# Optimization experiments

Measured on AMD Instinct MI355X. Metric: run time of the kernel, lower is better.

Reference implementation:

```python
import jax, jax.numpy as jnp
import numpy as np

HEADS = 8
NEG = -1e9
EPS = 1e-9


def setup_inputs() -> dict:
    key = jax.random.key(0)
    ks = jax.random.split(key, 24)
    N, D, E = 2048, 512, 64
    s = 0.02
    inp = {
        "xyz": jax.random.normal(ks[0], (N, 3), jnp.float32),
        "str_feat": jax.random.normal(ks[1], (N, D), jnp.float32),
        "esm_feat": jax.random.normal(ks[2], (N, E), jnp.float32),
        "y_hat": jax.random.uniform(ks[3], (N, 1), jnp.float32),
        "distance_mask": jax.random.randint(ks[4], (N, N), 0, 2, jnp.int32),
        "t": jnp.ones((1,), jnp.float32),
        "band_width": jnp.ones((1,), jnp.float32),
        "max_iter": 5,
        # main projections (torch Linear layout: y = x @ W.T + b)
        "Wq": jax.random.normal(ks[5], (D, D), jnp.float32) * s,
        "bq": jnp.zeros((D,), jnp.float32),
        "Wk": jax.random.normal(ks[6], (D, D), jnp.float32) * s,
        "bk": jnp.zeros((D,), jnp.float32),
        "Wv": jax.random.normal(ks[7], (D, D), jnp.float32) * s,
        "bv": jnp.zeros((D,), jnp.float32),
        "Wo": jax.random.normal(ks[8], (D, D), jnp.float32) * s,
        "bo": jnp.zeros((D,), jnp.float32),
        # esm projections (computed in the original forward but unused downstream)
        "Weq": jax.random.normal(ks[9], (E, E), jnp.float32) * s,
        "beq": jnp.zeros((E,), jnp.float32),
        "Wek": jax.random.normal(ks[10], (E, E), jnp.float32) * s,
        "bek": jnp.zeros((E,), jnp.float32),
        "Wev": jax.random.normal(ks[11], (E, E), jnp.float32) * s,
        "bev": jnp.zeros((E,), jnp.float32),
        "Weo": jax.random.normal(ks[12], (E, E), jnp.float32) * s,
        "beo": jnp.zeros((E,), jnp.float32),
    }
    return inp


def reference(xyz, str_feat, esm_feat, y_hat, distance_mask, t, band_width, max_iter,
              Wq, bq, Wk, bk, Wv, bv, Wo, bo,
              Weq, beq, Wek, bek, Wev, bev, Weo, beo):
    N, D = str_feat.shape
    h = HEADS
    dh = D // h

    q = str_feat @ Wq.T + bq
    k = str_feat @ Wk.T + bk
    v = str_feat @ Wv.T + bv
    # esm projections: computed in the original forward but never used (dead code; DCE'd under jit)
    _esm_q = esm_feat @ Weq.T + beq
    _esm_k = esm_feat @ Wek.T + bek
    _esm_v = esm_feat @ Wev.T + bev

    # [h, N, dh]
    qh = q.reshape(N, h, dh).transpose(1, 0, 2)
    kh = k.reshape(N, h, dh).transpose(1, 0, 2)
    vh = v.reshape(N, h, dh).transpose(1, 0, 2)

    scores = jnp.einsum('hnd,hmd->hnm', qh, kh) / jnp.sqrt(jnp.asarray(dh, qh.dtype))
    mask = (distance_mask > 0)[None]              # [1, N, N]
    yw = y_hat[:, 0][None, :]                     # [1, N] per-target weight
    inv_two_bw2 = 1.0 / (2.0 * band_width[0] ** 2)
    temp = t[0]

    def step(carry, _):
        xyz_c, _x = carry
        # squared pairwise distances via the expanded form (avoids [N,N,3])
        sq = jnp.sum(xyz_c * xyz_c, axis=-1)
        d2 = sq[:, None] + sq[None, :] - 2.0 * (xyz_c @ xyz_c.T)
        kern = jnp.exp(-d2 * inv_two_bw2)          # [N, N] band-width kernel
        logits = scores / temp + jnp.log(kern * yw + EPS)[None]
        logits = jnp.where(mask, logits, NEG)
        attn = jax.nn.softmax(logits, axis=-1)     # [h, N, N]
        xyz_new = jnp.einsum('nm,md->nd', attn.mean(0), xyz_c)  # mean-shift step
        x_new = jnp.einsum('hnm,hmd->hnd', attn, vh)            # [h, N, dh]
        return (xyz_new, x_new), None

    (xyz_out, xh), _ = jax.lax.scan(step, (xyz, jnp.zeros_like(vh)), None, length=max_iter)
    x = xh.transpose(1, 0, 2).reshape(N, D)
    out = x @ Wo.T + bo
    return xyz_out, out
```

## Files before the change

kernel.cpp:

```cpp
#include <hip/hip_runtime.h>


typedef __attribute__((ext_vector_type(8))) short bf16x8;
typedef __attribute__((ext_vector_type(4))) short bf16x4;
typedef __attribute__((ext_vector_type(4))) float f32x4;
typedef __attribute__((ext_vector_type(4))) int   i32x4;

__device__ __forceinline__ unsigned short f2bf(float f) {
    unsigned int u = __float_as_uint(f);
    u += 0x7fff + ((u >> 16) & 1);
    return (unsigned short)(u >> 16);
}
__device__ __forceinline__ float bf2f(unsigned short u) {
    return __uint_as_float((unsigned int)u << 16);
}

union EU  { bf16x8 v; i32x4 i; unsigned short u[8]; };
union EU4 { bf16x4 v; unsigned short u[4]; };

__global__ __launch_bounds__(256)
void conv_all(const float* __restrict__ strf,
              const float* __restrict__ Wq, const float* __restrict__ Wk,
              const float* __restrict__ Wv, const int* __restrict__ dmask,
              unsigned short* __restrict__ sA, unsigned short* __restrict__ sW,
              unsigned char* __restrict__ mby)
{
    const long base = (long)(blockIdx.x * 256 + threadIdx.x) * 8;
    if (base >= 1048576 + 786432) {
        const long rel = base - (1048576 + 786432);
        int4 a = *reinterpret_cast<const int4*>(dmask + rel);
        int4 b = *reinterpret_cast<const int4*>(dmask + rel + 4);
        unsigned long long p = 0;
        p |= (a.x > 0) ? 0x01ULL : 0;  p |= (a.y > 0) ? 0x0100ULL : 0;
        p |= (a.z > 0) ? 0x010000ULL : 0;  p |= (a.w > 0) ? 0x01000000ULL : 0;
        p |= (b.x > 0) ? 0x0100000000ULL : 0;  p |= (b.y > 0) ? 0x010000000000ULL : 0;
        p |= (b.z > 0) ? 0x01000000000000ULL : 0;  p |= (b.w > 0) ? 0x0100000000000000ULL : 0;
        *reinterpret_cast<unsigned long long*>(mby + rel) = p;
        return;
    }
    const float* src;
    unsigned short* dst;
    if (base < 1048576) {
        src = strf + base; dst = sA + base;
    } else {
        const long rel = base - 1048576;
        const int seg = (int)(rel >> 18);
        const long off = rel & 262143;
        src = (seg == 0 ? Wq : (seg == 1 ? Wk : Wv)) + off;
        dst = sW + (long)seg * 262144 + off;
    }
    float4 a = *reinterpret_cast<const float4*>(src);
    float4 b = *reinterpret_cast<const float4*>(src + 4);
    EU o;
    o.u[0] = f2bf(a.x); o.u[1] = f2bf(a.y); o.u[2] = f2bf(a.z); o.u[3] = f2bf(a.w);
    o.u[4] = f2bf(b.x); o.u[5] = f2bf(b.y); o.u[6] = f2bf(b.z); o.u[7] = f2bf(b.w);
    *reinterpret_cast<bf16x8*>(dst) = o.v;
}

__global__ __launch_bounds__(256)
void qkv_mfma(const unsigned short* __restrict__ sA,
              const unsigned short* __restrict__ sW,
              const float* __restrict__ bq, const float* __restrict__ bk,
              const float* __restrict__ bv,
              unsigned short* __restrict__ qh, unsigned short* __restrict__ kh,
              unsigned short* __restrict__ vT)
{
    const int z  = blockIdx.z;
    const int bx = blockIdx.x;
    const int by = blockIdx.y;
    const int tid = threadIdx.x;
    const int wv = tid >> 6;
    const int lane = tid & 63;
    const int row  = lane & 15;
    const int koct = (lane >> 4) * 8;
    const int n0 = bx * 64;

    const unsigned short* Ap = sA + (long)(n0 + wv * 16 + row) * 512;
    const unsigned short* Bp = sW + (long)z * 262144 + (long)(by * 64 + row) * 512;

    f32x4 acc[4] = {};
#pragma unroll
    for (int k0 = 0; k0 < 512; k0 += 32) {
        bf16x8 a = *reinterpret_cast<const bf16x8*>(Ap + k0 + koct);
#pragma unroll
        for (int t = 0; t < 4; t++) {
            bf16x8 b = *reinterpret_cast<const bf16x8*>(Bp + (long)(t * 16) * 512 + k0 + koct);
            acc[t] = __builtin_amdgcn_mfma_f32_16x16x32_bf16(a, b, acc[t], 0, 0, 0);
        }
    }

    if (z == 2) {
        const int rbase = n0 + wv * 16 + (lane >> 4) * 4;
#pragma unroll
        for (int t = 0; t < 4; t++) {
            const int d = by * 64 + t * 16 + (lane & 15);
            const float bb = bv[d];
            ushort4 o;
            o.x = f2bf(acc[t][0] + bb); o.y = f2bf(acc[t][1] + bb);
            o.z = f2bf(acc[t][2] + bb); o.w = f2bf(acc[t][3] + bb);
            *reinterpret_cast<ushort4*>(vT + (long)d * 2048 + rbase) = o;
        }
        return;
    }

    __shared__ float ls[64][68];
    const int lrb = wv * 16 + (lane >> 4) * 4;
    const int lcb = lane & 15;
#pragma unroll
    for (int t = 0; t < 4; t++)
#pragma unroll
        for (int r = 0; r < 4; r++)
            ls[lrb + r][t * 16 + lcb] = acc[t][r];
    __syncthreads();

    const float* bias = (z == 0) ? bq : bk;
    unsigned short* dst = (z == 0) ? qh : kh;
    const int r2 = tid >> 2;
    const int c2 = (tid & 3) * 16;
    float sv[16];
#pragma unroll
    for (int j = 0; j < 4; j++) {
        float4 s = *reinterpret_cast<const float4*>(&ls[r2][c2 + j * 4]);
        float4 bb = *reinterpret_cast<const float4*>(bias + by * 64 + c2 + j * 4);
        sv[j*4+0] = s.x + bb.x; sv[j*4+1] = s.y + bb.y;
        sv[j*4+2] = s.z + bb.z; sv[j*4+3] = s.w + bb.w;
    }
    EU o0, o1;
#pragma unroll
    for (int j = 0; j < 8; j++) { o0.u[j] = f2bf(sv[j]); o1.u[j] = f2bf(sv[8 + j]); }
    unsigned short* dp = dst + (long)(n0 + r2) * 512 + by * 64 + c2;
    *reinterpret_cast<bf16x8*>(dp)     = o0.v;
    *reinterpret_cast<bf16x8*>(dp + 8) = o1.v;
}

__global__ __launch_bounds__(256)
void scores_mfma(const unsigned short* __restrict__ qh,
                 const unsigned short* __restrict__ kh,
                 const unsigned char* __restrict__ mby,
                 const float* __restrict__ tptr,
                 unsigned short* __restrict__ Ebf)
{
    const int h  = blockIdx.z;
    const int m0 = blockIdx.x * 128;
    const int n0 = blockIdx.y * 64;
    const int tid = threadIdx.x;
    const int wv = tid >> 6;
    const int lane = tid & 63;
    const float scale = 1.0f / (8.0f * tptr[0]);

    const int row  = lane & 15;
    const int koct = (lane >> 4) * 8;
    const unsigned short* Aq = qh + (long)(n0 + wv * 16 + row) * 512 + h * 64;
    const unsigned short* Bk = kh + (long)(m0 + row) * 512 + h * 64;

    f32x4 acc[8] = {};
#pragma unroll
    for (int k0 = 0; k0 < 64; k0 += 32) {
        bf16x8 a = *reinterpret_cast<const bf16x8*>(Aq + k0 + koct);
#pragma unroll
        for (int t = 0; t < 8; t++) {
            bf16x8 b = *reinterpret_cast<const bf16x8*>(Bk + (long)(t * 16) * 512 + k0 + koct);
            acc[t] = __builtin_amdgcn_mfma_f32_16x16x32_bf16(a, b, acc[t], 0, 0, 0);
        }
    }

    __shared__ unsigned short lsb[4][16][140];
    const int rr = (lane >> 4) * 4;
    const int cc = lane & 15;
#pragma unroll
    for (int t = 0; t < 8; t++)
#pragma unroll
        for (int r = 0; r < 4; r++)
            lsb[wv][rr + r][t * 16 + cc] = f2bf(__expf(acc[t][r] * scale));

    const int rr2 = lane >> 2;
    const int c32 = (lane & 3) * 32;
    const int gn  = n0 + wv * 16 + rr2;

    EU4 ev[8];
#pragma unroll
    for (int j = 0; j < 8; j++)
        ev[j].v = *reinterpret_cast<const bf16x4*>(&lsb[wv][rr2][c32 + 4 * j]);

    union MB { uint4 q; unsigned char b[16]; } mb0, mb1;
    const unsigned char* mrow = mby + (long)gn * 2048 + m0 + c32;
    mb0.q = *reinterpret_cast<const uint4*>(mrow);
    mb1.q = *reinterpret_cast<const uint4*>(mrow + 16);

    EU o[4];
#pragma unroll
    for (int e = 0; e < 32; e++) {
        const unsigned char mk = (e < 16) ? mb0.b[e] : mb1.b[e - 16];
        o[e >> 3].u[e & 7] = mk ? ev[e >> 2].u[e & 3] : (unsigned short)0;
    }
    unsigned short* ep = Ebf + (long)gn * 16384 + h * 2048 + m0 + c32;
#pragma unroll
    for (int t = 0; t < 4; t++)
        *reinterpret_cast<bf16x8*>(ep + t * 8) = o[t].v;
}

__global__ __launch_bounds__(256)
void ms_iter(const unsigned short* __restrict__ Ebf,
             const float* __restrict__ xyz_src,
             float* __restrict__ xyz_dst,
             const float* __restrict__ y_hat,
             const float* __restrict__ bwp,
             unsigned short* __restrict__ attn_out,
             int write_attn)
{
    const int n = blockIdx.x;
    const int tid = threadIdx.x;
    const int lane = tid & 63;
    const int wave = tid >> 6;
    const int m0 = tid * 8;

    __shared__ float red[64];

    EU E[8];
    const i32x4* Epv = reinterpret_cast<const i32x4*>(Ebf + (long)n * 16384 + m0);
#pragma unroll
    for (int h = 0; h < 8; h++)
        E[h].i = __builtin_nontemporal_load(Epv + h * 256);

    const float bw = bwp[0];
    const float c2k = 1.0f / (2.0f * bw * bw);

    const float xn = xyz_src[n * 3 + 0];
    const float yn = xyz_src[n * 3 + 1];
    const float zn = xyz_src[n * 3 + 2];
    const float sqn = xn * xn + yn * yn + zn * zn;

    float mx[8], my[8], mz[8];
    {
        const float4* xp = reinterpret_cast<const float4*>(xyz_src + (long)m0 * 3);
        float4 a = xp[0], b = xp[1], c = xp[2], d = xp[3], e = xp[4], f = xp[5];
        mx[0]=a.x; my[0]=a.y; mz[0]=a.z;  mx[1]=a.w; my[1]=b.x; mz[1]=b.y;
        mx[2]=b.z; my[2]=b.w; mz[2]=c.x;  mx[3]=c.y; my[3]=c.z; mz[3]=c.w;
        mx[4]=d.x; my[4]=d.y; mz[4]=d.z;  mx[5]=d.w; my[5]=e.x; mz[5]=e.y;
        mx[6]=e.z; my[6]=e.w; mz[6]=f.x;  mx[7]=f.y; my[7]=f.z; mz[7]=f.w;
    }
    float4 yh0 = *reinterpret_cast<const float4*>(y_hat + m0);
    float4 yh1 = *reinterpret_cast<const float4*>(y_hat + m0 + 4);
    float yh[8] = {yh0.x, yh0.y, yh0.z, yh0.w, yh1.x, yh1.y, yh1.z, yh1.w};

    float g[8];
#pragma unroll
    for (int j = 0; j < 8; j++) {
        const float d2 = sqn + (mx[j]*mx[j] + my[j]*my[j] + mz[j]*mz[j])
                       - 2.0f * (xn*mx[j] + yn*my[j] + zn*mz[j]);
        g[j] = __expf(-d2 * c2k) * yh[j] + 1e-9f;
    }

    float z[8];
#pragma unroll
    for (int h = 0; h < 8; h++) {
        float zz = 0.f;
#pragma unroll
        for (int j = 0; j < 8; j++) zz += bf2f(E[h].u[j]) * g[j];
        z[h] = zz;
    }

#pragma unroll
    for (int h = 0; h < 8; h++) {
        float v = z[h];
#pragma unroll
        for (int off = 32; off > 0; off >>= 1) v += __shfl_down(v, off, 64);
        if (lane == 0) red[wave * 8 + h] = v;
    }
    __syncthreads();
    if (tid < 8) {
        const float s = red[tid] + red[8 + tid] + red[16 + tid] + red[24 + tid];
        red[32 + tid] = 1.0f / s;
    }
    __syncthreads();
    float invz[8];
#pragma unroll
    for (int h = 0; h < 8; h++) invz[h] = red[32 + h];
    __syncthreads();

    float ax = 0.f, ay = 0.f, az = 0.f;
#pragma unroll
    for (int j = 0; j < 8; j++) {
        float w = 0.f;
#pragma unroll
        for (int h = 0; h < 8; h++) w += bf2f(E[h].u[j]) * invz[h];
        w *= 0.125f * g[j];
        ax += w * mx[j]; ay += w * my[j]; az += w * mz[j];
    }
    if (write_attn) {
        unsigned short* ap = attn_out + (long)n * 16384 + m0;
#pragma unroll
        for (int h = 0; h < 8; h++) {
            EU o;
#pragma unroll
            for (int j = 0; j < 8; j++)
                o.u[j] = f2bf(bf2f(E[h].u[j]) * g[j] * invz[h]);
            *reinterpret_cast<bf16x8*>(ap + h * 2048) = o.v;
        }
    }

    float v3[3] = {ax, ay, az};
#pragma unroll
    for (int c = 0; c < 3; c++) {
        float v = v3[c];
#pragma unroll
        for (int off = 32; off > 0; off >>= 1) v += __shfl_down(v, off, 64);
        if (lane == 0) red[c * 4 + wave] = v;
    }
    __syncthreads();
    if (tid < 3) {
        xyz_dst[n * 3 + tid] = red[tid * 4 + 0] + red[tid * 4 + 1] +
                               red[tid * 4 + 2] + red[tid * 4 + 3];
    }
}

__global__ __launch_bounds__(256)
void av_mfma(const unsigned short* __restrict__ attn,
             const unsigned short* __restrict__ vT,
             float* __restrict__ xb)
{
    const int h  = blockIdx.z;
    const int s  = blockIdx.y;
    const int bx = blockIdx.x;
    const int wv = threadIdx.x >> 6;
    const int lane = threadIdx.x & 63;
    const int n0 = bx * 64 + wv * 16;
    const int kc = s * 512;

    const int mrow = lane & 15;
    const int koct = (lane >> 4) * 8;

    const unsigned short* Ab = attn + (long)(n0 + mrow) * 16384 + h * 2048;
    const unsigned short* Bb = vT + ((long)h * 64 + mrow) * 2048;

    f32x4 acc[4] = {};
    for (int k0 = kc; k0 < kc + 512; k0 += 32) {
        EU au;
        au.i = __builtin_nontemporal_load(reinterpret_cast<const i32x4*>(Ab + k0 + koct));
#pragma unroll
        for (int t = 0; t < 4; t++) {
            bf16x8 b = *reinterpret_cast<const bf16x8*>(Bb + (long)(t * 16) * 2048 + k0 + koct);
            acc[t] = __builtin_amdgcn_mfma_f32_16x16x32_bf16(au.v, b, acc[t], 0, 0, 0);
        }
    }

    const int rbase = n0 + (lane >> 4) * 4;
    const int dcol = lane & 15;
#pragma unroll
    for (int t = 0; t < 4; t++)
#pragma unroll
        for (int r = 0; r < 4; r++)
            atomicAdd(&xb[(long)(rbase + r) * 512 + h * 64 + t * 16 + dcol], acc[t][r]);
}

__global__ __launch_bounds__(256)
void gemm_nt(const float* __restrict__ A,
             const float* __restrict__ B,
             const float* __restrict__ bias,
             float* __restrict__ C)
{
    __shared__ float As[16][68];
    __shared__ float Bs[16][68];

    const int tid = threadIdx.x;
    const int i0 = blockIdx.x * 64;
    const int j0 = blockIdx.y * 64;
    const int tx = tid & 15, ty = tid >> 4;
    const int lr = tid >> 2;
    const int lc = (tid & 3) << 2;

    float acc[4][4] = {};

    for (int k0 = 0; k0 < 512; k0 += 16) {
        float4 av = *reinterpret_cast<const float4*>(A + (long)(i0 + lr) * 512 + (k0 + lc));
        float4 bv = *reinterpret_cast<const float4*>(B + (long)(j0 + lr) * 512 + (k0 + lc));
        As[lc + 0][lr] = av.x; As[lc + 1][lr] = av.y; As[lc + 2][lr] = av.z; As[lc + 3][lr] = av.w;
        Bs[lc + 0][lr] = bv.x; Bs[lc + 1][lr] = bv.y; Bs[lc + 2][lr] = bv.z; Bs[lc + 3][lr] = bv.w;
        __syncthreads();
#pragma unroll
        for (int kk = 0; kk < 16; kk++) {
            float4 a = *reinterpret_cast<const float4*>(&As[kk][ty << 2]);
            float4 b = *reinterpret_cast<const float4*>(&Bs[kk][tx << 2]);
            float ar[4] = {a.x, a.y, a.z, a.w};
            float br[4] = {b.x, b.y, b.z, b.w};
#pragma unroll
            for (int p = 0; p < 4; p++)
#pragma unroll
                for (int q = 0; q < 4; q++)
                    acc[p][q] += ar[p] * br[q];
        }
        __syncthreads();
    }

#pragma unroll
    for (int p = 0; p < 4; p++) {
        const int row = i0 + (ty << 2) + p;
        const int col = j0 + (tx << 2);
        float4 o;
        o.x = acc[p][0] + bias[col + 0];
        o.y = acc[p][1] + bias[col + 1];
        o.z = acc[p][2] + bias[col + 2];
        o.w = acc[p][3] + bias[col + 3];
        *reinterpret_cast<float4*>(C + (long)row * 512 + col) = o;
    }
}

extern "C" void kernel_launch(void* const* d_in, const int* in_sizes, int n_in,
                              void* d_out, int out_size, void* d_ws, size_t ws_size,
                              hipStream_t stream)
{
    (void)in_sizes; (void)n_in; (void)out_size; (void)ws_size;

    const float* xyz   = (const float*)d_in[0];
    const float* strf  = (const float*)d_in[1];
    const float* yhat  = (const float*)d_in[3];
    const int*   dmask = (const int*)d_in[4];
    const float* tptr  = (const float*)d_in[5];
    const float* bwptr = (const float*)d_in[6];
    const float* Wq = (const float*)d_in[8];
    const float* bq = (const float*)d_in[9];
    const float* Wk = (const float*)d_in[10];
    const float* bk = (const float*)d_in[11];
    const float* Wv = (const float*)d_in[12];
    const float* bv = (const float*)d_in[13];
    const float* Wo = (const float*)d_in[14];
    const float* bo = (const float*)d_in[15];
    float* outp = (float*)d_out;

    char* wsb = (char*)d_ws;
    float* xb            = (float*)(wsb);
    unsigned short* sA   = (unsigned short*)(wsb + (4L << 20));
    unsigned short* sW   = (unsigned short*)(wsb + (6L << 20));
    unsigned short* qh   = (unsigned short*)(wsb + (8L << 20));
    unsigned short* kh   = (unsigned short*)(wsb + (10L << 20));
    unsigned short* vT   = (unsigned short*)(wsb + (12L << 20));
    float* xyzA          = (float*)(wsb + (14L << 20));
    float* xyzB          = xyzA + 8192;
    unsigned short* Ebf  = (unsigned short*)(wsb + (16L << 20));
    unsigned char* mby   = (unsigned char*)(wsb + (80L << 20));

    dim3 blk(256, 1, 1);

    conv_all<<<dim3(2944), blk, 0, stream>>>(strf, Wq, Wk, Wv, dmask, sA, sW, mby);
    qkv_mfma<<<dim3(32, 8, 3), blk, 0, stream>>>(sA, sW, bq, bk, bv, qh, kh, vT);

    scores_mfma<<<dim3(16, 32, 8), blk, 0, stream>>>(qh, kh, mby, tptr, Ebf);

    const float* src = xyz;
    float* dsts[5] = {xyzA, xyzB, xyzA, xyzB, outp};
    for (int it = 0; it < 5; it++) {
        ms_iter<<<dim3(2048), blk, 0, stream>>>(Ebf, src, dsts[it], yhat, bwptr,
                                                Ebf, it == 4 ? 1 : 0);
        src = dsts[it];
    }

    hipMemsetAsync(xb, 0, 2048L * 512 * sizeof(float), stream);
    av_mfma<<<dim3(32, 4, 8), blk, 0, stream>>>(Ebf, vT, xb);

    gemm_nt<<<dim3(32, 8, 1), blk, 0, stream>>>(xb, Wo, bo, outp + 6144);
}
```

Before: 387.0 us.

## Reorganize attention layout head-major, replace atomics and fp32 output GEMM with MFMA

The E/attention buffer moves from [n][h][m] to head-major [h][n][m]. The scores kernel is rewritten so each block covers 16 query rows across all keys for one head. The atomicAdd split-K accumulation in av_mfma is replaced by per-split partial buffers plus a reduction kernel that writes bf16. The fp32 SIMT output GEMM becomes a bf16 MFMA GEMM, with Wo converted in conv_all. Together these remove the memset and atomics and speed up the final projection, at the cost of extra partial-buffer traffic and bf16 rounding of the attention output before Wo.

Result: faster. 368.3 us (-4.8%).

```diff
diff --git a/kernel.cpp b/kernel.cpp
--- a/kernel.cpp
+++ b/kernel.cpp
@@ -2,9 +2,7 @@
 
 
 typedef __attribute__((ext_vector_type(8))) short bf16x8;
-typedef __attribute__((ext_vector_type(4))) short bf16x4;
 typedef __attribute__((ext_vector_type(4))) float f32x4;
-typedef __attribute__((ext_vector_type(4))) int   i32x4;
 
 __device__ __forceinline__ unsigned short f2bf(float f) {
     unsigned int u = __float_as_uint(f);
@@ -15,19 +13,19 @@
     return __uint_as_float((unsigned int)u << 16);
 }
 
-union EU  { bf16x8 v; i32x4 i; unsigned short u[8]; };
-union EU4 { bf16x4 v; unsigned short u[4]; };
+union EU { bf16x8 v; unsigned short u[8]; };
 
 __global__ __launch_bounds__(256)
 void conv_all(const float* __restrict__ strf,
               const float* __restrict__ Wq, const float* __restrict__ Wk,
-              const float* __restrict__ Wv, const int* __restrict__ dmask,
+              const float* __restrict__ Wv, const float* __restrict__ Wo,
+              const int* __restrict__ dmask,
               unsigned short* __restrict__ sA, unsigned short* __restrict__ sW,
               unsigned char* __restrict__ mby)
 {
     const long base = (long)(blockIdx.x * 256 + threadIdx.x) * 8;
-    if (base >= 1048576 + 786432) {
-        const long rel = base - (1048576 + 786432);
+    if (base >= 2097152) {
+        const long rel = base - 2097152;
         int4 a = *reinterpret_cast<const int4*>(dmask + rel);
         int4 b = *reinterpret_cast<const int4*>(dmask + rel + 4);
         unsigned long long p = 0;
@@ -46,7 +44,8 @@
         const long rel = base - 1048576;
         const int seg = (int)(rel >> 18);
         const long off = rel & 262143;
-        src = (seg == 0 ? Wq : (seg == 1 ? Wk : Wv)) + off;
+        const float* Ws[4] = {Wq, Wk, Wv, Wo};
+        src = Ws[seg] + off;
         dst = sW + (long)seg * 262144 + off;
     }
     float4 a = *reinterpret_cast<const float4*>(src);
@@ -134,69 +133,64 @@
 }
 
 __global__ __launch_bounds__(256)
-void scores_mfma(const unsigned short* __restrict__ qh,
+void scores_rows(const unsigned short* __restrict__ qh,
                  const unsigned short* __restrict__ kh,
                  const unsigned char* __restrict__ mby,
                  const float* __restrict__ tptr,
                  unsigned short* __restrict__ Ebf)
 {
-    const int h  = blockIdx.z;
-    const int m0 = blockIdx.x * 128;
-    const int n0 = blockIdx.y * 64;
+    const int h  = blockIdx.y;
+    const int n0 = blockIdx.x * 16;
     const int tid = threadIdx.x;
     const int wv = tid >> 6;
     const int lane = tid & 63;
     const float scale = 1.0f / (8.0f * tptr[0]);
 
-    const int row  = lane & 15;
+    __shared__ unsigned short lsb[4][16][268];
+
+    const int arow = lane & 15;
     const int koct = (lane >> 4) * 8;
-    const unsigned short* Aq = qh + (long)(n0 + wv * 16 + row) * 512 + h * 64;
-    const unsigned short* Bk = kh + (long)(m0 + row) * 512 + h * 64;
-
-    f32x4 acc[8] = {};
-#pragma unroll
-    for (int k0 = 0; k0 < 64; k0 += 32) {
-        bf16x8 a = *reinterpret_cast<const bf16x8*>(Aq + k0 + koct);
-#pragma unroll
-        for (int t = 0; t < 8; t++) {
-            bf16x8 b = *reinterpret_cast<const bf16x8*>(Bk + (long)(t * 16) * 512 + k0 + koct);
-            acc[t] = __builtin_amdgcn_mfma_f32_16x16x32_bf16(a, b, acc[t], 0, 0, 0);
-        }
-    }
-
-    __shared__ unsigned short lsb[4][16][140];
-    const int rr = (lane >> 4) * 4;
-    const int cc = lane & 15;
-#pragma unroll
-    for (int t = 0; t < 8; t++)
-#pragma unroll
-        for (int r = 0; r < 4; r++)
-            lsb[wv][rr + r][t * 16 + cc] = f2bf(__expf(acc[t][r] * scale));
-
-    const int rr2 = lane >> 2;
-    const int c32 = (lane & 3) * 32;
-    const int gn  = n0 + wv * 16 + rr2;
-
-    EU4 ev[8];
-#pragma unroll
-    for (int j = 0; j < 8; j++)
-        ev[j].v = *reinterpret_cast<const bf16x4*>(&lsb[wv][rr2][c32 + 4 * j]);
-
-    union MB { uint4 q; unsigned char b[16]; } mb0, mb1;
-    const unsigned char* mrow = mby + (long)gn * 2048 + m0 + c32;
-    mb0.q = *reinterpret_cast<const uint4*>(mrow);
-    mb1.q = *reinterpret_cast<const uint4*>(mrow + 16);
-
-    EU o[4];
-#pragma unroll
-    for (int e = 0; e < 32; e++) {
-        const unsigned char mk = (e < 16) ? mb0.b[e] : mb1.b[e - 16];
-        o[e >> 3].u[e & 7] = mk ? ev[e >> 2].u[e & 3] : (unsigned short)0;
-    }
-    unsigned short* ep = Ebf + (long)gn * 16384 + h * 2048 + m0 + c32;
-#pragma unroll
-    for (int t = 0; t < 4; t++)
-        *reinterpret_cast<bf16x8*>(ep + t * 8) = o[t].v;
+    const unsigned short* Aq = qh + (long)(n0 + arow) * 512 + h * 64;
+    const bf16x8 aq0 = *reinterpret_cast<const bf16x8*>(Aq + koct);
+    const bf16x8 aq1 = *reinterpret_cast<const bf16x8*>(Aq + 32 + koct);
+
+    const int lr = (lane >> 4) * 4;
+    const int lc = lane & 15;
+    const int rrd = lane & 15;
+    const int cgr = (lane >> 4) * 64;
+
+#pragma unroll
+    for (int half = 0; half < 2; half++) {
+        const int mbase = wv * 512 + half * 256;
+#pragma unroll
+        for (int mt = 0; mt < 16; mt++) {
+            const int m0 = mbase + mt * 16;
+            const unsigned short* Bk = kh + (long)(m0 + arow) * 512 + h * 64;
+            bf16x8 b0 = *reinterpret_cast<const bf16x8*>(Bk + koct);
+            bf16x8 b1 = *reinterpret_cast<const bf16x8*>(Bk + 32 + koct);
+            f32x4 c = {};
+            c = __builtin_amdgcn_mfma_f32_16x16x32_bf16(aq0, b0, c, 0, 0, 0);
+            c = __builtin_amdgcn_mfma_f32_16x16x32_bf16(aq1, b1, c, 0, 0, 0);
+#pragma unroll
+            for (int r = 0; r < 4; r++)
+                lsb[wv][lr + r][mt * 16 + lc] = f2bf(__expf(c[r] * scale));
+        }
+        const int gn = n0 + rrd;
+        const int mabs = mbase + cgr;
+        const unsigned char* mp = mby + (long)gn * 2048 + mabs;
+        unsigned short* ep = Ebf + ((long)h * 2048 + gn) * 2048 + mabs;
+#pragma unroll
+        for (int c8 = 0; c8 < 8; c8++) {
+            EU e;
+            e.v = *reinterpret_cast<const bf16x8*>(&lsb[wv][rrd][cgr + c8 * 8]);
+            unsigned long long mk = *reinterpret_cast<const unsigned long long*>(mp + c8 * 8);
+            EU o;
+#pragma unroll
+            for (int j = 0; j < 8; j++)
+                o.u[j] = ((mk >> (8 * j)) & 0xff) ? e.u[j] : (unsigned short)0;
+            *reinterpret_cast<bf16x8*>(ep + c8 * 8) = o.v;
+        }
+    }
 }
 
 __global__ __launch_bounds__(256)
@@ -217,10 +211,9 @@
     __shared__ float red[64];
 
     EU E[8];
-    const i32x4* Epv = reinterpret_cast<const i32x4*>(Ebf + (long)n * 16384 + m0);
 #pragma unroll
     for (int h = 0; h < 8; h++)
-        E[h].i = __builtin_nontemporal_load(Epv + h * 256);
+        E[h].v = *reinterpret_cast<const bf16x8*>(Ebf + (long)h * 4194304 + (long)n * 2048 + m0);
 
     const float bw = bwp[0];
     const float c2k = 1.0f / (2.0f * bw * bw);
@@ -288,14 +281,13 @@
         ax += w * mx[j]; ay += w * my[j]; az += w * mz[j];
     }
     if (write_attn) {
-        unsigned short* ap = attn_out + (long)n * 16384 + m0;
 #pragma unroll
         for (int h = 0; h < 8; h++) {
             EU o;
 #pragma unroll
             for (int j = 0; j < 8; j++)
                 o.u[j] = f2bf(bf2f(E[h].u[j]) * g[j] * invz[h]);
-            *reinterpret_cast<bf16x8*>(ap + h * 2048) = o.v;
+            *reinterpret_cast<bf16x8*>(attn_out + (long)h * 4194304 + (long)n * 2048 + m0) = o.v;
         }
     }
 
@@ -317,7 +309,7 @@
 __global__ __launch_bounds__(256)
 void av_mfma(const unsigned short* __restrict__ attn,
              const unsigned short* __restrict__ vT,
-             float* __restrict__ xb)
+             float* __restrict__ P)
 {
     const int h  = blockIdx.z;
     const int s  = blockIdx.y;
@@ -330,78 +322,85 @@
     const int mrow = lane & 15;
     const int koct = (lane >> 4) * 8;
 
-    const unsigned short* Ab = attn + (long)(n0 + mrow) * 16384 + h * 2048;
+    const unsigned short* Ab = attn + (long)h * 4194304 + (long)(n0 + mrow) * 2048;
     const unsigned short* Bb = vT + ((long)h * 64 + mrow) * 2048;
 
     f32x4 acc[4] = {};
     for (int k0 = kc; k0 < kc + 512; k0 += 32) {
-        EU au;
-        au.i = __builtin_nontemporal_load(reinterpret_cast<const i32x4*>(Ab + k0 + koct));
+        bf16x8 a = *reinterpret_cast<const bf16x8*>(Ab + k0 + koct);
 #pragma unroll
         for (int t = 0; t < 4; t++) {
             bf16x8 b = *reinterpret_cast<const bf16x8*>(Bb + (long)(t * 16) * 2048 + k0 + koct);
-            acc[t] = __builtin_amdgcn_mfma_f32_16x16x32_bf16(au.v, b, acc[t], 0, 0, 0);
-        }
-    }
-
+            acc[t] = __builtin_amdgcn_mfma_f32_16x16x32_bf16(a, b, acc[t], 0, 0, 0);
+        }
+    }
+
+    float* Pp = P + (long)s * 1048576;
     const int rbase = n0 + (lane >> 4) * 4;
     const int dcol = lane & 15;
 #pragma unroll
     for (int t = 0; t < 4; t++)
 #pragma unroll
         for (int r = 0; r < 4; r++)
-            atomicAdd(&xb[(long)(rbase + r) * 512 + h * 64 + t * 16 + dcol], acc[t][r]);
-}
-
-__global__ __launch_bounds__(256)
-void gemm_nt(const float* __restrict__ A,
-             const float* __restrict__ B,
-             const float* __restrict__ bias,
-             float* __restrict__ C)
-{
-    __shared__ float As[16][68];
-    __shared__ float Bs[16][68];
-
-    const int tid = threadIdx.x;
-    const int i0 = blockIdx.x * 64;
-    const int j0 = blockIdx.y * 64;
-    const int tx = tid & 15, ty = tid >> 4;
-    const int lr = tid >> 2;
-    const int lc = (tid & 3) << 2;
-
-    float acc[4][4] = {};
-
-    for (int k0 = 0; k0 < 512; k0 += 16) {
-        float4 av = *reinterpret_cast<const float4*>(A + (long)(i0 + lr) * 512 + (k0 + lc));
-        float4 bv = *reinterpret_cast<const float4*>(B + (long)(j0 + lr) * 512 + (k0 + lc));
-        As[lc + 0][lr] = av.x; As[lc + 1][lr] = av.y; As[lc + 2][lr] = av.z; As[lc + 3][lr] = av.w;
-        Bs[lc + 0][lr] = bv.x; Bs[lc + 1][lr] = bv.y; Bs[lc + 2][lr] = bv.z; Bs[lc + 3][lr] = bv.w;
-        __syncthreads();
-#pragma unroll
-        for (int kk = 0; kk < 16; kk++) {
-            float4 a = *reinterpret_cast<const float4*>(&As[kk][ty << 2]);
-            float4 b = *reinterpret_cast<const float4*>(&Bs[kk][tx << 2]);
-            float ar[4] = {a.x, a.y, a.z, a.w};
-            float br[4] = {b.x, b.y, b.z, b.w};
-#pragma unroll
-            for (int p = 0; p < 4; p++)
-#pragma unroll
-                for (int q = 0; q < 4; q++)
-                    acc[p][q] += ar[p] * br[q];
-        }
-        __syncthreads();
-    }
-
+            Pp[(long)(rbase + r) * 512 + h * 64 + t * 16 + dcol] = acc[t][r];
+}
+
+__global__ __launch_bounds__(256)
+void av_red(const float* __restrict__ P, unsigned short* __restrict__ xc)
+{
+    const long idx = (long)(blockIdx.x * 256 + threadIdx.x) * 8;
+    float s[8] = {};
 #pragma unroll
     for (int p = 0; p < 4; p++) {
-        const int row = i0 + (ty << 2) + p;
-        const int col = j0 + (tx << 2);
-        float4 o;
-        o.x = acc[p][0] + bias[col + 0];
-        o.y = acc[p][1] + bias[col + 1];
-        o.z = acc[p][2] + bias[col + 2];
-        o.w = acc[p][3] + bias[col + 3];
-        *reinterpret_cast<float4*>(C + (long)row * 512 + col) = o;
+        const float* pp = P + (long)p * 1048576 + idx;
+        float4 a = *reinterpret_cast<const float4*>(pp);
+        float4 b = *reinterpret_cast<const float4*>(pp + 4);
+        s[0] += a.x; s[1] += a.y; s[2] += a.z; s[3] += a.w;
+        s[4] += b.x; s[5] += b.y; s[6] += b.z; s[7] += b.w;
+    }
+    EU o;
+#pragma unroll
+    for (int j = 0; j < 8; j++) o.u[j] = f2bf(s[j]);
+    *reinterpret_cast<bf16x8*>(xc + idx) = o.v;
+}
+
+__global__ __launch_bounds__(256)
+void out_mfma(const unsigned short* __restrict__ xc,
+              const unsigned short* __restrict__ sW,
+              const float* __restrict__ bo,
+              float* __restrict__ out)
+{
+    const int bx = blockIdx.x;
+    const int by = blockIdx.y;
+    const int wv = threadIdx.x >> 6;
+    const int lane = threadIdx.x & 63;
+    const int row  = lane & 15;
+    const int koct = (lane >> 4) * 8;
+    const int n0 = bx * 64;
+
+    const unsigned short* Ap = xc + (long)(n0 + wv * 16 + row) * 512;
+    const unsigned short* Bp = sW + 3L * 262144 + (long)(by * 64 + row) * 512;
+
+    f32x4 acc[4] = {};
+#pragma unroll
+    for (int k0 = 0; k0 < 512; k0 += 32) {
+        bf16x8 a = *reinterpret_cast<const bf16x8*>(Ap + k0 + koct);
+#pragma unroll
+        for (int t = 0; t < 4; t++) {
+            bf16x8 b = *reinterpret_cast<const bf16x8*>(Bp + (long)(t * 16) * 512 + k0 + koct);
+            acc[t] = __builtin_amdgcn_mfma_f32_16x16x32_bf16(a, b, acc[t], 0, 0, 0);
+        }
+    }
+
+    const int rbase = n0 + wv * 16 + (lane >> 4) * 4;
+    const int dcol = lane & 15;
+#pragma unroll
+    for (int t = 0; t < 4; t++) {
+        const int col = by * 64 + t * 16 + dcol;
+        const float bb = bo[col];
+#pragma unroll
+        for (int r = 0; r < 4; r++)
+            out[(long)(rbase + r) * 512 + col] = acc[t][r] + bb;
     }
 }
 
@@ -428,23 +427,24 @@
     float* outp = (float*)d_out;
 
     char* wsb = (char*)d_ws;
-    float* xb            = (float*)(wsb);
-    unsigned short* sA   = (unsigned short*)(wsb + (4L << 20));
-    unsigned short* sW   = (unsigned short*)(wsb + (6L << 20));
-    unsigned short* qh   = (unsigned short*)(wsb + (8L << 20));
-    unsigned short* kh   = (unsigned short*)(wsb + (10L << 20));
-    unsigned short* vT   = (unsigned short*)(wsb + (12L << 20));
-    float* xyzA          = (float*)(wsb + (14L << 20));
+    float* Ppart         = (float*)(wsb);
+    unsigned short* xc   = (unsigned short*)(wsb + (16L << 20));
+    unsigned short* sA   = (unsigned short*)(wsb + (18L << 20));
+    unsigned short* sW   = (unsigned short*)(wsb + (20L << 20));
+    unsigned short* qh   = (unsigned short*)(wsb + (22L << 20));
+    unsigned short* kh   = (unsigned short*)(wsb + (24L << 20));
+    unsigned short* vT   = (unsigned short*)(wsb + (26L << 20));
+    float* xyzA          = (float*)(wsb + (28L << 20));
     float* xyzB          = xyzA + 8192;
-    unsigned short* Ebf  = (unsigned short*)(wsb + (16L << 20));
-    unsigned char* mby   = (unsigned char*)(wsb + (80L << 20));
+    unsigned char* mby   = (unsigned char*)(wsb + (30L << 20));
+    unsigned short* Ebf  = (unsigned short*)(wsb + (34L << 20));
 
     dim3 blk(256, 1, 1);
 
-    conv_all<<<dim3(2944), blk, 0, stream>>>(strf, Wq, Wk, Wv, dmask, sA, sW, mby);
+    conv_all<<<dim3(3072), blk, 0, stream>>>(strf, Wq, Wk, Wv, Wo, dmask, sA, sW, mby);
     qkv_mfma<<<dim3(32, 8, 3), blk, 0, stream>>>(sA, sW, bq, bk, bv, qh, kh, vT);
 
-    scores_mfma<<<dim3(16, 32, 8), blk, 0, stream>>>(qh, kh, mby, tptr, Ebf);
+    scores_rows<<<dim3(128, 8), blk, 0, stream>>>(qh, kh, mby, tptr, Ebf);
 
     const float* src = xyz;
     float* dsts[5] = {xyzA, xyzB, xyzA, xyzB, outp};
@@ -454,8 +454,7 @@
         src = dsts[it];
     }
 
-    hipMemsetAsync(xb, 0, 2048L * 512 * sizeof(float), stream);
-    av_mfma<<<dim3(32, 4, 8), blk, 0, stream>>>(Ebf, vT, xb);
-
-    gemm_nt<<<dim3(32, 8, 1), blk, 0, stream>>>(xb, Wo, bo, outp + 6144);
-}
+    av_mfma<<<dim3(32, 4, 8), blk, 0, stream>>>(Ebf, vT, Ppart);
+    av_red<<<dim3(512), blk, 0, stream>>>(Ppart, xc);
+    out_mfma<<<dim3(32, 8), blk, 0, stream>>>(xc, sW, bo, outp + 6144);
+}
```
